# Kernel optimization log

Hardware: AMD Instinct MI355X
Metric: run time of the kernel (lower is better)

## Reference

```python
import jax, jax.numpy as jnp
import numpy as np

VOCAB = 128
HID = 1024
STD = 0.01


def setup_inputs() -> dict:
    key = jax.random.key(0)
    ks = jax.random.split(key, 9)
    X = jax.random.randint(ks[0], (64, 512), 0, VOCAB, dtype=jnp.int32)
    def w(k, shape):
        return jax.random.normal(k, shape, dtype=jnp.float32) * STD
    return {
        "X": X,
        # reset gate
        "Wr_x": w(ks[1], (VOCAB, HID)), "Wr_h": w(ks[2], (HID, HID)), "b_r": jnp.zeros(HID, jnp.float32),
        # update gate
        "Wz_x": w(ks[3], (VOCAB, HID)), "Wz_h": w(ks[4], (HID, HID)), "b_z": jnp.zeros(HID, jnp.float32),
        # candidate
        "Wh_x": w(ks[5], (VOCAB, HID)), "Wh_h": w(ks[6], (HID, HID)), "b_h": jnp.zeros(HID, jnp.float32),
        # output head
        "W_o": w(ks[7], (HID, VOCAB)), "b_o": jnp.zeros(VOCAB, jnp.float32),
    }


def reference(X, Wr_x, Wr_h, b_r, Wz_x, Wz_h, b_z, Wh_x, Wh_h, b_h, W_o, b_o):
    B, T = X.shape
    # one-hot encode all timesteps: (T, B, V)
    Xoh = jax.nn.one_hot(X.T, VOCAB, dtype=jnp.float32)

    def step(h, x_t):
        # x_t: (B, V), h: (B, H)
        r = jax.nn.sigmoid(x_t @ Wr_x + h @ Wr_h + b_r)
        z = jax.nn.sigmoid(x_t @ Wz_x + h @ Wz_h + b_z)
        h_tilde = jnp.tanh(x_t @ Wh_x + (r * h) @ Wh_h + b_h)
        h_new = z * h + (1.0 - z) * h_tilde
        out = h_new @ W_o + b_o  # (B, V)
        return h_new, out

    h0 = jnp.zeros((B, HID), jnp.float32)
    _, outs = jax.lax.scan(step, h0, Xoh)  # outs: (T, B, V)
    return jnp.transpose(outs, (1, 0, 2))  # (B, T, V)
```

## Files before the change

kernel.cpp:

```cpp
#include <hip/hip_runtime.h>

#define HID   1024
#define TLEN  512
#define VOC   128
#define NBLK  256
#define NW    32
#define NO    2
#define LDSK  1032
#define HBUF  (64 * HID)
#define OD    16

typedef __bf16 bf16_t;
typedef __attribute__((ext_vector_type(8))) __bf16 bf16x8;
typedef __attribute__((ext_vector_type(4))) float  f32x4;
typedef __attribute__((ext_vector_type(2))) float  f32x2;
typedef __attribute__((ext_vector_type(4))) unsigned uint4v;

__device__ __forceinline__ float sigmoid_fast(float x) {
  return 1.0f / (1.0f + __expf(-x));
}
__device__ __forceinline__ float tanh_fast(float x) {
  float e = __expf(-2.0f * x);
  return (1.0f - e) / (1.0f + e);
}

union PairU { bf16_t b[2]; unsigned u; };

__device__ __forceinline__ void l1_inv() {
  asm volatile("buffer_inv" ::: "memory");
}

__device__ __forceinline__ void st_sc1(bf16_t* p, float f0, float f1) {
  PairU c; c.b[0] = (bf16_t)f0; c.b[1] = (bf16_t)f1;
  __hip_atomic_store((unsigned*)p, c.u, __ATOMIC_RELAXED, __HIP_MEMORY_SCOPE_AGENT);
}
__device__ __forceinline__ bf16x8 ld_nt16(const bf16_t* p) {
  union { uint4v u; bf16x8 b; } c;
  c.u = __builtin_nontemporal_load((const uint4v*)p);
  return c.b;
}

__device__ __forceinline__ void wait_local(const unsigned* lfl, int n, unsigned tgt) {
  if ((threadIdx.x >> 6) == 0) {
    const int lane = threadIdx.x & 63;
    for (;;) {
      l1_inv();
      unsigned g = tgt;
      if (lane < n)
        g = *(volatile const unsigned*)&lfl[lane];
      if (__all(g >= tgt)) break;
    }
  }
  __syncthreads();
}

__device__ __forceinline__ void wait_out_mall(const unsigned* oc0, const unsigned* oc1,
                                              unsigned otgt) {
  if ((threadIdx.x >> 6) == 0) {
    const int lane = threadIdx.x & 63;
    for (;;) {
      bool ok = true;
      if (lane == 0)      ok = __hip_atomic_load(oc0, __ATOMIC_RELAXED, __HIP_MEMORY_SCOPE_AGENT) >= otgt;
      else if (lane == 1) ok = __hip_atomic_load(oc1, __ATOMIC_RELAXED, __HIP_MEMORY_SCOPE_AGENT) >= otgt;
      if (__all(ok)) break;
      __builtin_amdgcn_s_sleep(1);
    }
  }
  __syncthreads();
}

__device__ __forceinline__ void wait1(const unsigned* ctr, unsigned tgt) {
  if (threadIdx.x == 0) {
    while (__hip_atomic_load(ctr, __ATOMIC_RELAXED, __HIP_MEMORY_SCOPE_AGENT) < tgt)
      __builtin_amdgcn_s_sleep(1);
  }
  __syncthreads();
}

#define MFMA(a, b, c) __builtin_amdgcn_mfma_f32_16x16x32_bf16((a), (b), (c), 0, 0, 0)

__global__ void __launch_bounds__(256, 1)
gru_lfl(const int* __restrict__ X,
        const float* __restrict__ Wr_x, const float* __restrict__ Wr_h, const float* __restrict__ b_r,
        const float* __restrict__ Wz_x, const float* __restrict__ Wz_h, const float* __restrict__ b_z,
        const float* __restrict__ Wh_x, const float* __restrict__ Wh_h, const float* __restrict__ b_h,
        const float* __restrict__ W_o,  const float* __restrict__ b_o,
        float* __restrict__ out,
        bf16_t* __restrict__ hring, bf16_t* __restrict__ rh_bf,
        bf16_t* __restrict__ oring, bf16_t* __restrict__ wz_bf,
        unsigned* __restrict__ flags, unsigned* __restrict__ lflags)
{
  __shared__ __align__(16) bf16_t Wbuf[2 * 32 * LDSK];
  __shared__ int s_role;

  unsigned* h_ctr  = flags;
  unsigned* oc0    = flags + 64;
  unsigned* oc1    = flags + 96;
  unsigned* cnt    = flags + 128;
  unsigned* winner = flags + 160;
  unsigned* ocnt   = flags + 164;
  unsigned* winv   = flags + 168;

  unsigned* lhf = lflags;
  unsigned* lrf = lflags + 64;

  const int tid  = threadIdx.x;
  const int lane = tid & 63;
  const int wv   = tid >> 6;
  const int n16  = lane & 15;
  const int q    = lane >> 4;
  const int aoff = (wv * 16 + n16) * HID + q * 8;

  int bi[4];
#pragma unroll
  for (int i = 0; i < 4; ++i) bi[i] = wv * 16 + q * 4 + i;

  if (tid == 0) {
    unsigned xcc;
    asm volatile("s_getreg_b32 %0, hwreg(HW_REG_XCC_ID)" : "=s"(xcc));
    xcc &= 7u;
    unsigned idx = __hip_atomic_fetch_add(&cnt[xcc], 1u, __ATOMIC_RELAXED, __HIP_MEMORY_SCOPE_AGENT);
    if (idx == NW - 1) {
      unsigned exp = 0u;
      __hip_atomic_compare_exchange_strong(winner, &exp, xcc + 1u,
          __ATOMIC_RELAXED, __ATOMIC_RELAXED, __HIP_MEMORY_SCOPE_AGENT);
    }
    unsigned w;
    do {
      w = __hip_atomic_load(winner, __ATOMIC_RELAXED, __HIP_MEMORY_SCOPE_AGENT);
      __builtin_amdgcn_s_sleep(1);
    } while (w == 0u);
    if (xcc == w - 1u && idx < NW) {
      s_role = (int)idx;
    } else {
      unsigned o = __hip_atomic_fetch_add(ocnt, 1u, __ATOMIC_RELAXED, __HIP_MEMORY_SCOPE_AGENT);
      s_role = (o < NO) ? (NW + (int)o) : -1;
    }
  }
  __syncthreads();
  const int role = s_role;
  if (role < 0) return;

  if (role < NW) {
    __builtin_amdgcn_fence(__ATOMIC_ACQUIRE, "agent");
    if (tid == 0) {
      __hip_atomic_fetch_add(winv, 1u, __ATOMIC_RELAXED, __HIP_MEMORY_SCOPE_AGENT);
      while (__hip_atomic_load(winv, __ATOMIC_RELAXED, __HIP_MEMORY_SCOPE_AGENT) < NW)
        __builtin_amdgcn_s_sleep(1);
    }
    __syncthreads();

    const int s  = role;
    const int c0 = s * 32;
    for (int idx = tid; idx < 32 * HID; idx += 256) {
      int n = idx & 31, k = idx >> 5;
      int r = (n & 1) * 16 + (n >> 1);
      Wbuf[r * LDSK + k]             = (bf16_t)Wr_h[k * HID + c0 + n];
      Wbuf[32 * LDSK + r * LDSK + k] = (bf16_t)Wh_h[k * HID + c0 + n];
    }
    bf16_t* wzs = wz_bf + s * (32 * 1024);
    for (int idx = tid; idx < 32 * HID; idx += 256) {
      int n = idx & 31, k = idx >> 5;
      int r = (n & 1) * 16 + (n >> 1);
      wzs[r * 1024 + k] = (bf16_t)Wz_h[k * HID + c0 + n];
    }

    const int j0 = c0 + 2 * n16;
#pragma unroll
    for (int i = 0; i < 4; ++i) {
      PairU zz; zz.b[0] = (bf16_t)0.f; zz.b[1] = (bf16_t)0.f;
      *reinterpret_cast<PairU*>(hring + bi[i] * HID + j0) = zz;
    }
    __syncthreads();
    if (tid == 0) {
      *(volatile unsigned*)&lhf[s] = 1u;
      __hip_atomic_fetch_add(h_ctr, 1u, __ATOMIC_RELAXED, __HIP_MEMORY_SCOPE_AGENT);
    }

    const float br0 = b_r[j0], br1 = b_r[j0 + 1];
    const float bz0 = b_z[j0], bz1 = b_z[j0 + 1];
    const float bh0 = b_h[j0], bh1 = b_h[j0 + 1];
    const bf16_t* wr0 = &Wbuf[n16 * LDSK + q * 8];
    const bf16_t* wr1 = &Wbuf[(16 + n16) * LDSK + q * 8];
    const bf16_t* wh0 = &Wbuf[32 * LDSK + n16 * LDSK + q * 8];
    const bf16_t* wh1 = &Wbuf[32 * LDSK + (16 + n16) * LDSK + q * 8];
    const bf16_t* wz0 = wzs + n16 * 1024 + q * 8;
    const bf16_t* wz1 = wzs + (16 + n16) * 1024 + q * 8;
    const bf16_t* rhrow = rh_bf + aoff;

    f32x4 hm0 = {0.f,0.f,0.f,0.f}, hm1 = {0.f,0.f,0.f,0.f};

    for (int t = 0; t < TLEN; ++t) {
      float gr0[4], gr1[4], gz0[4], gz1[4], gh0[4], gh1[4];
#pragma unroll
      for (int i = 0; i < 4; ++i) {
        int xb = X[bi[i] * TLEN + t];
        gr0[i] = Wr_x[xb * HID + j0]; gr1[i] = Wr_x[xb * HID + j0 + 1];
        gz0[i] = Wz_x[xb * HID + j0]; gz1[i] = Wz_x[xb * HID + j0 + 1];
        gh0[i] = Wh_x[xb * HID + j0]; gh1[i] = Wh_x[xb * HID + j0 + 1];
      }
      wait_local(lhf, NW, (unsigned)(t + 1));
      const bf16_t* hslot = hring + (t & 1) * HBUF;
      const bf16_t* hrow  = hslot + aoff;
      bf16x8 areg[32];
#pragma unroll
      for (int kk = 0; kk < 32; ++kk)
        areg[kk] = *reinterpret_cast<const bf16x8*>(hrow + kk * 32);
      f32x4 aR0 = {0.f,0.f,0.f,0.f}, aR1 = {0.f,0.f,0.f,0.f};
#pragma unroll
      for (int kk = 0; kk < 32; ++kk) {
        bf16x8 w0 = *reinterpret_cast<const bf16x8*>(wr0 + kk * 32);
        bf16x8 w1 = *reinterpret_cast<const bf16x8*>(wr1 + kk * 32);
        aR0 = MFMA(areg[kk], w0, aR0);
        aR1 = MFMA(areg[kk], w1, aR1);
      }
#pragma unroll
      for (int i = 0; i < 4; ++i) {
        float r0 = sigmoid_fast(aR0[i] + br0 + gr0[i]);
        float r1 = sigmoid_fast(aR1[i] + br1 + gr1[i]);
        PairU hp = *reinterpret_cast<const PairU*>(hslot + bi[i] * HID + j0);
        PairU c;
        c.b[0] = (bf16_t)(r0 * (float)hp.b[0]);
        c.b[1] = (bf16_t)(r1 * (float)hp.b[1]);
        *reinterpret_cast<PairU*>(rh_bf + bi[i] * HID + j0) = c;
      }
      __syncthreads();
      if (tid == 0) *(volatile unsigned*)&lrf[s] = (unsigned)(t + 1);

      f32x4 aZ0 = {0.f,0.f,0.f,0.f}, aZ1 = {0.f,0.f,0.f,0.f};
#pragma unroll
      for (int kk = 0; kk < 32; ++kk) {
        bf16x8 w0 = *reinterpret_cast<const bf16x8*>(wz0 + kk * 32);
        bf16x8 w1 = *reinterpret_cast<const bf16x8*>(wz1 + kk * 32);
        aZ0 = MFMA(areg[kk], w0, aZ0);
        aZ1 = MFMA(areg[kk], w1, aZ1);
      }
      f32x4 z0, z1;
#pragma unroll
      for (int i = 0; i < 4; ++i) {
        z0[i] = sigmoid_fast(aZ0[i] + bz0 + gz0[i]);
        z1[i] = sigmoid_fast(aZ1[i] + bz1 + gz1[i]);
      }

      if ((t & 7) == 0 && t + 8 > OD)
        wait_out_mall(oc0, oc1, (unsigned)(t + 8 - OD));
      wait_local(lrf, NW, (unsigned)(t + 1));
      bf16x8 breg[32];
#pragma unroll
      for (int kk = 0; kk < 32; ++kk)
        breg[kk] = *reinterpret_cast<const bf16x8*>(rhrow + kk * 32);
      f32x4 aH0 = {0.f,0.f,0.f,0.f}, aH1 = {0.f,0.f,0.f,0.f};
#pragma unroll
      for (int kk = 0; kk < 32; ++kk) {
        bf16x8 w0 = *reinterpret_cast<const bf16x8*>(wh0 + kk * 32);
        bf16x8 w1 = *reinterpret_cast<const bf16x8*>(wh1 + kk * 32);
        aH0 = MFMA(breg[kk], w0, aH0);
        aH1 = MFMA(breg[kk], w1, aH1);
      }
      bf16_t* hnext = hring + ((t + 1) & 1) * HBUF;
      bf16_t* onext = oring + ((t + 1) % OD) * HBUF;
#pragma unroll
      for (int i = 0; i < 4; ++i) {
        float ht0 = tanh_fast(aH0[i] + bh0 + gh0[i]);
        float ht1 = tanh_fast(aH1[i] + bh1 + gh1[i]);
        float hn0 = z0[i] * hm0[i] + (1.f - z0[i]) * ht0;
        float hn1 = z1[i] * hm1[i] + (1.f - z1[i]) * ht1;
        hm0[i] = hn0; hm1[i] = hn1;
        PairU c; c.b[0] = (bf16_t)hn0; c.b[1] = (bf16_t)hn1;
        *reinterpret_cast<PairU*>(hnext + bi[i] * HID + j0) = c;
        st_sc1(onext + bi[i] * HID + j0, hn0, hn1);
      }
      __syncthreads();
      if (tid == 0) {
        *(volatile unsigned*)&lhf[s] = (unsigned)(t + 2);
        __hip_atomic_fetch_add(h_ctr, 1u, __ATOMIC_RELAXED, __HIP_MEMORY_SCOPE_AGENT);
      }
    }
    __builtin_amdgcn_fence(__ATOMIC_RELEASE, "agent");
  } else {
    const int ob  = role - NW;
    const int c0o = ob * 64;
    for (int idx = tid; idx < 64 * HID; idx += 256) {
      int n = idx & 63, k = idx >> 6;
      int g = n >> 5, m = n & 31;
      int r = g * 32 + (m & 1) * 16 + (m >> 1);
      Wbuf[r * LDSK + k] = (bf16_t)W_o[k * VOC + c0o + n];
    }
    __syncthreads();

    float bo[2][2];
#pragma unroll
    for (int g = 0; g < 2; ++g) {
      bo[g][0] = b_o[c0o + 32 * g + 2 * n16];
      bo[g][1] = b_o[c0o + 32 * g + 2 * n16 + 1];
    }
    const bf16_t* wo[2][2];
#pragma unroll
    for (int g = 0; g < 2; ++g)
#pragma unroll
      for (int h = 0; h < 2; ++h)
        wo[g][h] = &Wbuf[(g * 32 + h * 16 + n16) * LDSK + q * 8];

    unsigned* myoc = (ob == 0) ? oc0 : oc1;
    for (int t = 1; t <= TLEN; ++t) {
      wait1(h_ctr, (unsigned)(NW * (t + 1)));
      const bf16_t* hrow = oring + (t % OD) * HBUF + aoff;
      bf16x8 areg[32];
#pragma unroll
      for (int kk = 0; kk < 32; ++kk)
        areg[kk] = ld_nt16(hrow + kk * 32);
      f32x4 acc[2][2];
#pragma unroll
      for (int g = 0; g < 2; ++g)
#pragma unroll
        for (int h = 0; h < 2; ++h)
          acc[g][h] = (f32x4){0.f, 0.f, 0.f, 0.f};
#pragma unroll
      for (int kk = 0; kk < 32; ++kk) {
#pragma unroll
        for (int g = 0; g < 2; ++g) {
          bf16x8 w0 = *reinterpret_cast<const bf16x8*>(wo[g][0] + kk * 32);
          bf16x8 w1 = *reinterpret_cast<const bf16x8*>(wo[g][1] + kk * 32);
          acc[g][0] = MFMA(areg[kk], w0, acc[g][0]);
          acc[g][1] = MFMA(areg[kk], w1, acc[g][1]);
        }
      }
#pragma unroll
      for (int g = 0; g < 2; ++g) {
        const int j0 = c0o + 32 * g + 2 * n16;
#pragma unroll
        for (int i = 0; i < 4; ++i) {
          f32x2 v = {acc[g][0][i] + bo[g][0], acc[g][1][i] + bo[g][1]};
          *reinterpret_cast<f32x2*>(&out[(bi[i] * TLEN + (t - 1)) * VOC + j0]) = v;
        }
      }
      __syncthreads();
      if (tid == 0)
        __hip_atomic_store(myoc, (unsigned)t, __ATOMIC_RELAXED, __HIP_MEMORY_SCOPE_AGENT);
    }
  }
}

extern "C" void kernel_launch(void* const* d_in, const int* in_sizes, int n_in,
                              void* d_out, int out_size, void* d_ws, size_t ws_size,
                              hipStream_t stream) {
  const int*   X    = (const int*)d_in[0];
  const float* Wr_x = (const float*)d_in[1];
  const float* Wr_h = (const float*)d_in[2];
  const float* b_r  = (const float*)d_in[3];
  const float* Wz_x = (const float*)d_in[4];
  const float* Wz_h = (const float*)d_in[5];
  const float* b_z  = (const float*)d_in[6];
  const float* Wh_x = (const float*)d_in[7];
  const float* Wh_h = (const float*)d_in[8];
  const float* b_h  = (const float*)d_in[9];
  const float* W_o  = (const float*)d_in[10];
  const float* b_o  = (const float*)d_in[11];

  char* ws = (char*)d_ws;
  unsigned* flags  = (unsigned*)ws;
  unsigned* lflags = (unsigned*)(ws + 4096);
  bf16_t*   hring  = (bf16_t*)(ws + 8192);
  bf16_t*   rh_bf  = (bf16_t*)(ws + 8192 + 2 * HBUF * sizeof(bf16_t));
  bf16_t*   oring  = (bf16_t*)(ws + 8192 + 3 * HBUF * sizeof(bf16_t));
  bf16_t*   wz_bf  = (bf16_t*)(ws + 8192 + (3 + OD) * HBUF * sizeof(bf16_t));

  hipMemsetAsync(ws, 0, 8192, stream);

  gru_lfl<<<NBLK, 256, 0, stream>>>(
      X, Wr_x, Wr_h, b_r, Wz_x, Wz_h, b_z, Wh_x, Wh_h, b_h, W_o, b_o,
      (float*)d_out, hring, rh_bf, oring, wz_bf, flags, lflags);
}
```

Before: 8.606 ms.

## Replace block-level barriers with per-wave flag synchronization across workgroups

Each wave now owns its 16 batch rows and publishes and waits on its own per-wave flags (local h/rh flags, per-wave h counters, per-wave output counters), replacing __syncthreads plus a single-thread flag write with a vmcnt drain and a lane-0 store. The output-ring store is moved after the h publish so the recurrent critical path does not wait on the agent-scope store. The intent is to remove block-wide barrier stalls from the serial timestep chain so waves progress independently. The cost is more flag traffic, more spinning waves, and reliance on subtle memory-ordering correctness, with a flag layout that has to stay within the 8 KB memset region.

```diff
diff --git a/kernel.cpp b/kernel.cpp
--- a/kernel.cpp
+++ b/kernel.cpp
@@ -29,6 +29,9 @@
 __device__ __forceinline__ void l1_inv() {
   asm volatile("buffer_inv" ::: "memory");
 }
+__device__ __forceinline__ void wave_drain() {
+  asm volatile("s_waitcnt vmcnt(0)" ::: "memory");
+}
 
 __device__ __forceinline__ void st_sc1(bf16_t* p, float f0, float f1) {
   PairU c; c.b[0] = (bf16_t)f0; c.b[1] = (bf16_t)f1;
@@ -40,47 +43,26 @@
   return c.b;
 }
 
-__device__ __forceinline__ void wait_local(const unsigned* lfl, int n, unsigned tgt) {
-  if ((threadIdx.x >> 6) == 0) {
-    const int lane = threadIdx.x & 63;
-    for (;;) {
-      l1_inv();
-      unsigned g = tgt;
-      if (lane < n)
-        g = *(volatile const unsigned*)&lfl[lane];
-      if (__all(g >= tgt)) break;
-    }
+__device__ __forceinline__ void wait_wave(const unsigned* fb, unsigned tgt) {
+  const int lane = threadIdx.x & 63;
+  for (;;) {
+    l1_inv();
+    unsigned g = tgt;
+    if (lane < 32)
+      g = *(volatile const unsigned*)&fb[lane];
+    if (__all(g >= tgt)) break;
   }
-  __syncthreads();
-}
-
-__device__ __forceinline__ void wait_out_mall(const unsigned* oc0, const unsigned* oc1,
-                                              unsigned otgt) {
-  if ((threadIdx.x >> 6) == 0) {
-    const int lane = threadIdx.x & 63;
-    for (;;) {
-      bool ok = true;
-      if (lane == 0)      ok = __hip_atomic_load(oc0, __ATOMIC_RELAXED, __HIP_MEMORY_SCOPE_AGENT) >= otgt;
-      else if (lane == 1) ok = __hip_atomic_load(oc1, __ATOMIC_RELAXED, __HIP_MEMORY_SCOPE_AGENT) >= otgt;
-      if (__all(ok)) break;
-      __builtin_amdgcn_s_sleep(1);
-    }
-  }
-  __syncthreads();
-}
-
-__device__ __forceinline__ void wait1(const unsigned* ctr, unsigned tgt) {
-  if (threadIdx.x == 0) {
-    while (__hip_atomic_load(ctr, __ATOMIC_RELAXED, __HIP_MEMORY_SCOPE_AGENT) < tgt)
-      __builtin_amdgcn_s_sleep(1);
-  }
-  __syncthreads();
+}
+__device__ __forceinline__ void pub_wave(unsigned* f, unsigned v) {
+  wave_drain();
+  if ((threadIdx.x & 63) == 0)
+    *(volatile unsigned*)f = v;
 }
 
 #define MFMA(a, b, c) __builtin_amdgcn_mfma_f32_16x16x32_bf16((a), (b), (c), 0, 0, 0)
 
 __global__ void __launch_bounds__(256, 1)
-gru_lfl(const int* __restrict__ X,
+gru_wav(const int* __restrict__ X,
         const float* __restrict__ Wr_x, const float* __restrict__ Wr_h, const float* __restrict__ b_r,
         const float* __restrict__ Wz_x, const float* __restrict__ Wz_h, const float* __restrict__ b_z,
         const float* __restrict__ Wh_x, const float* __restrict__ Wh_h, const float* __restrict__ b_h,
@@ -93,16 +75,12 @@
   __shared__ __align__(16) bf16_t Wbuf[2 * 32 * LDSK];
   __shared__ int s_role;
 
-  unsigned* h_ctr  = flags;
-  unsigned* oc0    = flags + 64;
-  unsigned* oc1    = flags + 96;
-  unsigned* cnt    = flags + 128;
-  unsigned* winner = flags + 160;
-  unsigned* ocnt   = flags + 164;
-  unsigned* winv   = flags + 168;
-
-  unsigned* lhf = lflags;
-  unsigned* lrf = lflags + 64;
+  unsigned* hctr   = flags;
+  unsigned* oc     = flags + 128;
+  unsigned* cnt    = flags + 512;
+  unsigned* winner = flags + 552;
+  unsigned* ocnt   = flags + 556;
+  unsigned* winv   = flags + 560;
 
   const int tid  = threadIdx.x;
   const int lane = tid & 63;
@@ -110,6 +88,9 @@
   const int n16  = lane & 15;
   const int q    = lane >> 4;
   const int aoff = (wv * 16 + n16) * HID + q * 8;
+
+  unsigned* lhf = lflags + wv * 64;
+  unsigned* lrf = lflags + 256 + wv * 64;
 
   int bi[4];
 #pragma unroll
@@ -164,6 +145,7 @@
       int r = (n & 1) * 16 + (n >> 1);
       wzs[r * 1024 + k] = (bf16_t)Wz_h[k * HID + c0 + n];
     }
+    __syncthreads();
 
     const int j0 = c0 + 2 * n16;
 #pragma unroll
@@ -171,11 +153,9 @@
       PairU zz; zz.b[0] = (bf16_t)0.f; zz.b[1] = (bf16_t)0.f;
       *reinterpret_cast<PairU*>(hring + bi[i] * HID + j0) = zz;
     }
-    __syncthreads();
-    if (tid == 0) {
-      *(volatile unsigned*)&lhf[s] = 1u;
-      __hip_atomic_fetch_add(h_ctr, 1u, __ATOMIC_RELAXED, __HIP_MEMORY_SCOPE_AGENT);
-    }
+    pub_wave(&lhf[s], 1u);
+    if (lane == 0)
+      __hip_atomic_fetch_add(&hctr[wv * 32], 1u, __ATOMIC_RELAXED, __HIP_MEMORY_SCOPE_AGENT);
 
     const float br0 = b_r[j0], br1 = b_r[j0 + 1];
     const float bz0 = b_z[j0], bz1 = b_z[j0 + 1];
@@ -199,7 +179,7 @@
         gz0[i] = Wz_x[xb * HID + j0]; gz1[i] = Wz_x[xb * HID + j0 + 1];
         gh0[i] = Wh_x[xb * HID + j0]; gh1[i] = Wh_x[xb * HID + j0 + 1];
       }
-      wait_local(lhf, NW, (unsigned)(t + 1));
+      wait_wave(lhf, (unsigned)(t + 1));
       const bf16_t* hslot = hring + (t & 1) * HBUF;
       const bf16_t* hrow  = hslot + aoff;
       bf16x8 areg[32];
@@ -224,8 +204,7 @@
         c.b[1] = (bf16_t)(r1 * (float)hp.b[1]);
         *reinterpret_cast<PairU*>(rh_bf + bi[i] * HID + j0) = c;
       }
-      __syncthreads();
-      if (tid == 0) *(volatile unsigned*)&lrf[s] = (unsigned)(t + 1);
+      pub_wave(&lrf[s], (unsigned)(t + 1));
 
       f32x4 aZ0 = {0.f,0.f,0.f,0.f}, aZ1 = {0.f,0.f,0.f,0.f};
 #pragma unroll
@@ -242,9 +221,18 @@
         z1[i] = sigmoid_fast(aZ1[i] + bz1 + gz1[i]);
       }
 
-      if ((t & 7) == 0 && t + 8 > OD)
-        wait_out_mall(oc0, oc1, (unsigned)(t + 8 - OD));
-      wait_local(lrf, NW, (unsigned)(t + 1));
+      if ((t & 7) == 0 && t + 8 > OD) {
+        unsigned otgt = (unsigned)(t + 8 - OD);
+        for (;;) {
+          bool ok = true;
+          if (lane < NO)
+            ok = __hip_atomic_load(&oc[(lane * 4 + wv) * 32], __ATOMIC_RELAXED,
+                                   __HIP_MEMORY_SCOPE_AGENT) >= otgt;
+          if (__all(ok)) break;
+          __builtin_amdgcn_s_sleep(1);
+        }
+      }
+      wait_wave(lrf, (unsigned)(t + 1));
       bf16x8 breg[32];
 #pragma unroll
       for (int kk = 0; kk < 32; ++kk)
@@ -259,22 +247,24 @@
       }
       bf16_t* hnext = hring + ((t + 1) & 1) * HBUF;
       bf16_t* onext = oring + ((t + 1) % OD) * HBUF;
+      float hn0v[4], hn1v[4];
 #pragma unroll
       for (int i = 0; i < 4; ++i) {
         float ht0 = tanh_fast(aH0[i] + bh0 + gh0[i]);
         float ht1 = tanh_fast(aH1[i] + bh1 + gh1[i]);
         float hn0 = z0[i] * hm0[i] + (1.f - z0[i]) * ht0;
         float hn1 = z1[i] * hm1[i] + (1.f - z1[i]) * ht1;
-        hm0[i] = hn0; hm1[i] = hn1;
+        hm0[i] = hn0; hm1[i] = hn1; hn0v[i] = hn0; hn1v[i] = hn1;
         PairU c; c.b[0] = (bf16_t)hn0; c.b[1] = (bf16_t)hn1;
         *reinterpret_cast<PairU*>(hnext + bi[i] * HID + j0) = c;
-        st_sc1(onext + bi[i] * HID + j0, hn0, hn1);
-      }
-      __syncthreads();
-      if (tid == 0) {
-        *(volatile unsigned*)&lhf[s] = (unsigned)(t + 2);
-        __hip_atomic_fetch_add(h_ctr, 1u, __ATOMIC_RELAXED, __HIP_MEMORY_SCOPE_AGENT);
-      }
+      }
+      pub_wave(&lhf[s], (unsigned)(t + 2));
+#pragma unroll
+      for (int i = 0; i < 4; ++i)
+        st_sc1(onext + bi[i] * HID + j0, hn0v[i], hn1v[i]);
+      wave_drain();
+      if (lane == 0)
+        __hip_atomic_fetch_add(&hctr[wv * 32], 1u, __ATOMIC_RELAXED, __HIP_MEMORY_SCOPE_AGENT);
     }
     __builtin_amdgcn_fence(__ATOMIC_RELEASE, "agent");
   } else {
@@ -301,9 +291,16 @@
       for (int h = 0; h < 2; ++h)
         wo[g][h] = &Wbuf[(g * 32 + h * 16 + n16) * LDSK + q * 8];
 
-    unsigned* myoc = (ob == 0) ? oc0 : oc1;
+    unsigned* myhc = &hctr[wv * 32];
+    unsigned* myoc = &oc[(ob * 4 + wv) * 32];
     for (int t = 1; t <= TLEN; ++t) {
-      wait1(h_ctr, (unsigned)(NW * (t + 1)));
+      for (;;) {
+        unsigned g = 0xFFFFFFFFu;
+        if (lane == 0)
+          g = __hip_atomic_load(myhc, __ATOMIC_RELAXED, __HIP_MEMORY_SCOPE_AGENT);
+        if (__all(g >= (unsigned)(NW * (t + 1)))) break;
+        __builtin_amdgcn_s_sleep(1);
+      }
       const bf16_t* hrow = oring + (t % OD) * HBUF + aoff;
       bf16x8 areg[32];
 #pragma unroll
@@ -334,8 +331,8 @@
           *reinterpret_cast<f32x2*>(&out[(bi[i] * TLEN + (t - 1)) * VOC + j0]) = v;
         }
       }
-      __syncthreads();
-      if (tid == 0)
+      wave_drain();
+      if (lane == 0)
         __hip_atomic_store(myoc, (unsigned)t, __ATOMIC_RELAXED, __HIP_MEMORY_SCOPE_AGENT);
     }
   }
@@ -367,7 +364,7 @@
 
   hipMemsetAsync(ws, 0, 8192, stream);
 
-  gru_lfl<<<NBLK, 256, 0, stream>>>(
+  gru_wav<<<NBLK, 256, 0, stream>>>(
       X, Wr_x, Wr_h, b_r, Wz_x, Wz_h, b_z, Wh_x, Wh_h, b_h, W_o, b_o,
       (float*)d_out, hring, rh_bf, oring, wz_bf, flags, lflags);
 }
```

Result: slower. 8.786 ms (+2.1%).
